# Kernel tuning notes

Hardware: AMD Instinct MI355X
Metric: run time of the kernel (lower is better)

## Reference

```python
import jax, jax.numpy as jnp
import numpy as np
import math
from jax import lax

B, D, L, K, CONV_NUM, NH, DK = 8, 128, 1024, 7, 4, 8, 16


def _pos_encoding():
    i = np.arange(D, dtype=np.float64)
    freqs = np.where(i % 2 == 0, 10000.0 ** (-i / D), -(10000.0 ** (-(i - 1) / D)))
    phases = np.where(i % 2 == 0, 0.0, math.pi / 2)
    pos = np.arange(L, dtype=np.float64)
    pe = np.sin(pos[None, :] * freqs[:, None] + phases[:, None])  # [D, L]
    return jnp.asarray(pe, dtype=jnp.float32)


def setup_inputs() -> dict:
    key = jax.random.key(0)
    ks = jax.random.split(key, 10)
    x = jax.random.normal(ks[0], (B, D, L), dtype=jnp.float32)
    pos_enc = _pos_encoding()
    ln_w = jnp.ones((D, L), dtype=jnp.float32)   # LayerNorm([D, L]) weight
    ln_b = jnp.zeros((D, L), dtype=jnp.float32)  # LayerNorm([D, L]) bias
    dw = jax.random.normal(ks[1], (CONV_NUM, D, K), dtype=jnp.float32) * 0.1   # depthwise kernels
    pw = jax.random.normal(ks[2], (CONV_NUM, D, D), dtype=jnp.float32) * 0.08  # pointwise (1x1) kernels
    Wq = jax.random.normal(ks[3], (NH, B, DK, D), dtype=jnp.float32) * 0.08
    Wk = jax.random.normal(ks[4], (NH, B, DK, D), dtype=jnp.float32) * 0.08
    Wv = jax.random.normal(ks[5], (NH, B, DK, D), dtype=jnp.float32) * 0.08
    Wo = jax.random.normal(ks[6], (B, D, D), dtype=jnp.float32) * 0.08
    W = jax.random.normal(ks[7], (B, D, D), dtype=jnp.float32) * 0.08
    return {"x": x, "pos_enc": pos_enc, "ln_w": ln_w, "ln_b": ln_b,
            "dw": dw, "pw": pw, "Wq": Wq, "Wk": Wk, "Wv": Wv, "Wo": Wo, "W": W}


def _layernorm(y, w, b):
    # normalized over the last two dims [D, L] (matches nn.LayerNorm([D, L]))
    m = jnp.mean(y, axis=(1, 2), keepdims=True)
    v = jnp.var(y, axis=(1, 2), keepdims=True)
    return (y - m) / jnp.sqrt(v + 1e-5) * w + b


def _dsconv(y, dwk, pwk):
    # depthwise conv1d (groups=D, padding=K//2, no bias), then pointwise 1x1
    y = lax.conv_general_dilated(
        y, dwk[:, None, :], window_strides=(1,), padding=[(K // 2, K // 2)],
        feature_group_count=D, dimension_numbers=("NCH", "OIH", "NCH"))
    return jnp.einsum("oc,bcl->bol", pwk, y)


def _self_attention(x, Wq, Wk, Wv, Wo):
    inv = 1.0 / math.sqrt(DK)
    Q = jnp.einsum("hbdc,bcl->hbdl", Wq, x)  # [NH,B,DK,L]
    Kt = jnp.einsum("hbdc,bcl->hbdl", Wk, x)
    V = jnp.einsum("hbdc,bcl->hbdl", Wv, x)
    scores = jnp.einsum("hbdl,hbdm->hblm", Q, Kt) * inv  # [NH,B,L,L]
    # torch does F.softmax(out, dim=1) on [B,L,L] -> softmax over the first L axis
    A = jax.nn.softmax(scores, axis=2)
    heads = jnp.einsum("hbvl,hblm->hbvm", V, A)  # [NH,B,DV,L]
    head = jnp.transpose(heads, (1, 0, 2, 3)).reshape(B, NH * DK, L)  # concat along channel dim
    return jnp.einsum("bdc,bcl->bdl", Wo, head)


def reference(x, pos_enc, ln_w, ln_b, dw, pw, Wq, Wk, Wv, Wo, W):
    # dropout layers are identity (eval mode)
    out = x + pos_enc[None, :, :]
    res = out
    for i in range(CONV_NUM):
        out = _layernorm(out, ln_w, ln_b)
        out = _dsconv(out, dw[i], pw[i])
        out = jax.nn.relu(out)
        out = out + res
        res = out
        out = _layernorm(out, ln_w, ln_b)
    out = _self_attention(out, Wq, Wk, Wv, Wo)
    out = out + res
    res = out
    out = _layernorm(out, ln_w, ln_b)
    out = jnp.einsum("bdc,bcl->bdl", W, out)
    out = jax.nn.relu(out)
    out = out + res
    return out
```

## Files before the change

kernel.cpp:

```cpp
#include <hip/hip_runtime.h>
#include <hip/hip_bf16.h>

#define B_ 8
#define D_ 128
#define L_ 1024
#define KSZ 7
#define NH_ 8
#define DK_ 16

constexpr int BD = D_ * L_;
constexpr float LN_EPS = 1e-5f;
constexpr float INV_N = 1.0f / (float)BD;

typedef _Float16 half4 __attribute__((ext_vector_type(4)));
typedef float f32x4 __attribute__((ext_vector_type(4)));

template<int NS>
__device__ __forceinline__ void block_reduce_wave(float* s, float* redbuf, float* slot, int tid) {
    #pragma unroll
    for (int k = 0; k < NS; ++k) {
        float v = s[k];
        #pragma unroll
        for (int mk = 32; mk >= 1; mk >>= 1) v += __shfl_xor(v, mk, 64);
        s[k] = v;
    }
    int w = tid >> 6, lane = tid & 63;
    __syncthreads();
    if (lane == 0) {
        #pragma unroll
        for (int k = 0; k < NS; ++k) redbuf[w * NS + k] = s[k];
    }
    __syncthreads();
    if (tid == 0) {
        #pragma unroll
        for (int k = 0; k < NS; ++k)
            slot[k] = redbuf[k] + redbuf[NS + k] + redbuf[2 * NS + k] + redbuf[3 * NS + k];
    }
}

template<int LNMODE>
__device__ __forceinline__ void ln_stats_wave0(
    const float* __restrict__ pin, const float* __restrict__ wmom,
    int b, float* stat4, int tid)
{
    if (tid < 64) {
        float s0=0,s1=0,s2=0,s3=0,s4=0,s5=0,w0=0,w1=0,w2=0,w3=0,w4=0;
        const float* p = pin + (b * 64 + tid) * 8;
        s0 = p[0]; s1 = p[1];
        if constexpr (LNMODE == 2) {
            s2 = p[2]; s3 = p[3]; s4 = p[4]; s5 = p[5];
            const float* q = wmom + tid * 8;
            w0 = q[0]; w1 = q[1]; w2 = q[2]; w3 = q[3]; w4 = q[4];
        }
        #pragma unroll
        for (int mk = 32; mk >= 1; mk >>= 1) {
            s0 += __shfl_xor(s0, mk, 64); s1 += __shfl_xor(s1, mk, 64);
            if constexpr (LNMODE == 2) {
                s2 += __shfl_xor(s2, mk, 64); s3 += __shfl_xor(s3, mk, 64);
                s4 += __shfl_xor(s4, mk, 64); s5 += __shfl_xor(s5, mk, 64);
                w0 += __shfl_xor(w0, mk, 64); w1 += __shfl_xor(w1, mk, 64);
                w2 += __shfl_xor(w2, mk, 64); w3 += __shfl_xor(w3, mk, 64);
                w4 += __shfl_xor(w4, mk, 64);
            }
        }
        if (tid == 0) {
            float m1 = s0 * INV_N;
            float r1 = rsqrtf(s1 * INV_N - m1 * m1 + LN_EPS);
            stat4[0] = m1; stat4[1] = r1;
            if constexpr (LNMODE == 2) {
                float Sy  = r1 * (s2 - m1 * w0) + w2;
                float Sy2 = r1 * r1 * (s4 - 2.f * m1 * s3 + m1 * m1 * w1)
                          + 2.f * r1 * (s5 - m1 * w4) + w3;
                float m2 = Sy * INV_N;
                float r2 = rsqrtf(Sy2 * INV_N - m2 * m2 + LN_EPS);
                stat4[2] = m2; stat4[3] = r2;
            }
        }
    }
    __syncthreads();
}

__global__ __launch_bounds__(256) void k_addpos_wm(
    const float* __restrict__ x, const float* __restrict__ pos,
    const float* __restrict__ lnw, const float* __restrict__ lnb,
    float* __restrict__ out, float* __restrict__ part, float* __restrict__ wp)
{
    __shared__ float red[32];
    int b = blockIdx.y, blk = blockIdx.x, tid = threadIdx.x;
    if (b == 8) {
        int base = blk * 2048 + tid * 8;
        float s[5] = {0.f, 0.f, 0.f, 0.f, 0.f};
        #pragma unroll
        for (int q = 0; q < 2; ++q) {
            float4 wv = *(const float4*)(lnw + base + q * 4);
            float4 bv = *(const float4*)(lnb + base + q * 4);
            float wa[4] = {wv.x, wv.y, wv.z, wv.w};
            float ba[4] = {bv.x, bv.y, bv.z, bv.w};
            #pragma unroll
            for (int e = 0; e < 4; ++e) {
                float w = wa[e], bb = ba[e];
                s[0] += w; s[1] += w * w; s[2] += bb; s[3] += bb * bb; s[4] += w * bb;
            }
        }
        block_reduce_wave<5>(s, red, wp + blk * 8, tid);
        return;
    }
    int base = b * BD + blk * 2048;
    const float4* x4 = (const float4*)(x + base);
    const float4* p4 = (const float4*)(pos + blk * 2048);
    float4* o4 = (float4*)(out + base);
    float s[2] = {0.f, 0.f};
    #pragma unroll
    for (int j = 0; j < 2; ++j) {
        int idx = j * 256 + tid;
        float4 xv = x4[idx], pv = p4[idx];
        float4 r = {xv.x + pv.x, xv.y + pv.y, xv.z + pv.z, xv.w + pv.w};
        o4[idx] = r;
        s[0] += r.x + r.y + r.z + r.w;
        s[1] += r.x * r.x + r.y * r.y + r.z * r.z + r.w * r.w;
    }
    block_reduce_wave<2>(s, red, part + (b * 64 + blk) * 8, tid);
}

template<int LNMODE>
__global__ __launch_bounds__(256) void k_convblock(
    const float* __restrict__ src, const float* __restrict__ lnw, const float* __restrict__ lnb,
    const float* __restrict__ dwk, const float* __restrict__ pwk,
    const float* __restrict__ wmom, const float* __restrict__ pin,
    float* __restrict__ outbuf, float* __restrict__ pout)
{
    constexpr int XSTR = 136;
    constexpr int CSTR = 20;
    __shared__ _Float16 Xt[16 * XSTR];
    __shared__ float Ct[128 * CSTR];
    __shared__ float stat4[4];
    __shared__ float red[32];
    int lt = blockIdx.x, b = blockIdx.y;
    int tid = threadIdx.x;
    int l0 = lt * 16;

    ln_stats_wave0<LNMODE>(pin, wmom, b, stat4, tid);
    float m1 = stat4[0], r1 = stat4[1];
    float m2 = 0.f, r2 = 1.f;
    if constexpr (LNMODE == 2) { m2 = stat4[2]; r2 = stat4[3]; }

    {
        int c = tid >> 1, lh = tid & 1;
        int base = l0 + lh * 8;
        const float* srow = src + b * BD + c * L_;
        const float* wrow = lnw + c * L_;
        const float* brow = lnb + c * L_;
        float z[16];
        #pragma unroll
        for (int q = 0; q < 4; ++q) {
            int le = base - 4 + q * 4;
            if (le >= 0 && le <= L_ - 4) {
                float4 sv = *(const float4*)(srow + le);
                float4 wv = *(const float4*)(wrow + le);
                float4 bv = *(const float4*)(brow + le);
                float sa[4] = {sv.x, sv.y, sv.z, sv.w};
                float wa[4] = {wv.x, wv.y, wv.z, wv.w};
                float ba[4] = {bv.x, bv.y, bv.z, bv.w};
                #pragma unroll
                for (int e = 0; e < 4; ++e) {
                    float y = (sa[e] - m1) * r1 * wa[e] + ba[e];
                    if constexpr (LNMODE == 2) y = (y - m2) * r2 * wa[e] + ba[e];
                    z[q * 4 + e] = y;
                }
            } else {
                #pragma unroll
                for (int e = 0; e < 4; ++e) {
                    int l = le + e;
                    float zz = 0.f;
                    if (l >= 0 && l < L_) {
                        float y = (srow[l] - m1) * r1 * wrow[l] + brow[l];
                        if constexpr (LNMODE == 2) y = (y - m2) * r2 * wrow[l] + brow[l];
                        zz = y;
                    }
                    z[q * 4 + e] = zz;
                }
            }
        }
        float t0 = dwk[c*KSZ+0], t1 = dwk[c*KSZ+1], t2 = dwk[c*KSZ+2], t3 = dwk[c*KSZ+3],
              t4 = dwk[c*KSZ+4], t5 = dwk[c*KSZ+5], t6 = dwk[c*KSZ+6];
        #pragma unroll
        for (int j = 0; j < 8; ++j) {
            float o = t0*z[j+1] + t1*z[j+2] + t2*z[j+3] + t3*z[j+4]
                    + t4*z[j+5] + t5*z[j+6] + t6*z[j+7];
            Xt[(lh * 8 + j) * XSTR + c] = (_Float16)o;
        }
    }
    __syncthreads();

    int w = tid >> 6, lane = tid & 63, lg = lane >> 4, ln = lane & 15;
    int o0 = w * 32;
    const float* wrow0 = pwk + (o0 + ln) * D_;
    const float* wrow1 = pwk + (o0 + 16 + ln) * D_;
    f32x4 acc0 = {0.f, 0.f, 0.f, 0.f};
    f32x4 acc1 = {0.f, 0.f, 0.f, 0.f};
    #pragma unroll
    for (int kk = 0; kk < 8; ++kk) {
        float4 wv0 = *(const float4*)(wrow0 + kk * 16 + lg * 4);
        float4 wv1 = *(const float4*)(wrow1 + kk * 16 + lg * 4);
        half4 af0 = {(_Float16)wv0.x, (_Float16)wv0.y, (_Float16)wv0.z, (_Float16)wv0.w};
        half4 af1 = {(_Float16)wv1.x, (_Float16)wv1.y, (_Float16)wv1.z, (_Float16)wv1.w};
        half4 bf = *(const half4*)(&Xt[ln * XSTR + kk * 16 + lg * 4]);
        acc0 = __builtin_amdgcn_mfma_f32_16x16x16f16(af0, bf, acc0, 0, 0, 0);
        acc1 = __builtin_amdgcn_mfma_f32_16x16x16f16(af1, bf, acc1, 0, 0, 0);
    }

    #pragma unroll
    for (int om = 0; om < 2; ++om) {
        const f32x4& a = om ? acc1 : acc0;
        #pragma unroll
        for (int r = 0; r < 4; ++r)
            Ct[(o0 + om * 16 + lg * 4 + r) * CSTR + ln] = a[r];
    }
    __syncthreads();

    float s[6] = {0.f, 0.f, 0.f, 0.f, 0.f, 0.f};
    {
        int og = tid >> 1, hh = tid & 1;
        int lcol = l0 + hh * 8;
        int idx = b * BD + og * L_ + lcol;
        int widx = og * L_ + lcol;
        float4 c0 = *(const float4*)(&Ct[og * CSTR + hh * 8]);
        float4 c1 = *(const float4*)(&Ct[og * CSTR + hh * 8 + 4]);
        float4 rs0 = *(const float4*)(src + idx);
        float4 rs1 = *(const float4*)(src + idx + 4);
        float4 w0 = *(const float4*)(lnw + widx);
        float4 w1 = *(const float4*)(lnw + widx + 4);
        float4 b0 = *(const float4*)(lnb + widx);
        float4 b1 = *(const float4*)(lnb + widx + 4);
        float cv[8] = {c0.x, c0.y, c0.z, c0.w, c1.x, c1.y, c1.z, c1.w};
        float rv[8] = {rs0.x, rs0.y, rs0.z, rs0.w, rs1.x, rs1.y, rs1.z, rs1.w};
        float wv[8] = {w0.x, w0.y, w0.z, w0.w, w1.x, w1.y, w1.z, w1.w};
        float bv[8] = {b0.x, b0.y, b0.z, b0.w, b1.x, b1.y, b1.z, b1.w};
        float ov[8];
        #pragma unroll
        for (int e = 0; e < 8; ++e) {
            float v = fmaxf(cv[e], 0.f) + rv[e];
            ov[e] = v;
            float wvv = wv[e] * v;
            s[0] += v; s[1] += v * v; s[2] += wvv;
            s[3] += wv[e] * wvv; s[4] += wvv * wvv; s[5] += bv[e] * wvv;
        }
        *(float4*)(outbuf + idx)     = (float4){ov[0], ov[1], ov[2], ov[3]};
        *(float4*)(outbuf + idx + 4) = (float4){ov[4], ov[5], ov[6], ov[7]};
    }
    block_reduce_wave<6>(s, red, pout + (b * 64 + lt) * 8, tid);
}

template<bool LNSTAGE, int XSTR>
__device__ __forceinline__ void stage_tile(
    const float* __restrict__ X, const float* __restrict__ lnw, const float* __restrict__ lnb,
    _Float16* Xt, int b, int l0, float m1, float r1, int tid)
{
    int c = tid >> 1, lh = tid & 1;
    int off = c * L_ + l0 + lh * 16;
    const float* xp = X + b * BD + off;
    const float* wp = lnw + off;
    const float* bp = lnb + off;
    #pragma unroll
    for (int q = 0; q < 4; ++q) {
        float4 v = *(const float4*)(xp + q * 4);
        if constexpr (LNSTAGE) {
            float4 wv = *(const float4*)(wp + q * 4);
            float4 bv = *(const float4*)(bp + q * 4);
            v.x = (v.x - m1) * r1 * wv.x + bv.x;
            v.y = (v.y - m1) * r1 * wv.y + bv.y;
            v.z = (v.z - m1) * r1 * wv.z + bv.z;
            v.w = (v.w - m1) * r1 * wv.w + bv.w;
        }
        int lb_ = lh * 16 + q * 4;
        Xt[(lb_ + 0) * XSTR + c] = (_Float16)v.x;
        Xt[(lb_ + 1) * XSTR + c] = (_Float16)v.y;
        Xt[(lb_ + 2) * XSTR + c] = (_Float16)v.z;
        Xt[(lb_ + 3) * XSTR + c] = (_Float16)v.w;
    }
}

__global__ __launch_bounds__(256) void k_qkv(
    const float* __restrict__ Wq, const float* __restrict__ Wk, const float* __restrict__ Wv,
    const float* __restrict__ X, const float* __restrict__ lnw, const float* __restrict__ lnb,
    const float* __restrict__ pin,
    float* __restrict__ oq, float* __restrict__ ok, float* __restrict__ ov)
{
    constexpr int XSTR = 136;
    constexpr int CSTR = 36;
    __shared__ _Float16 Xt[32 * XSTR];
    __shared__ float Ct[64 * CSTR];
    __shared__ float stat4[4];
    int lt = blockIdx.x, rb = blockIdx.y, b = blockIdx.z;
    int tid = threadIdx.x;
    int l0 = lt * 32, r0 = rb * 64;

    ln_stats_wave0<1>(pin, nullptr, b, stat4, tid);
    stage_tile<true, XSTR>(X, lnw, lnb, Xt, b, l0, stat4[0], stat4[1], tid);
    __syncthreads();

    int w = tid >> 6, lane = tid & 63, lg = lane >> 4, ln = lane & 15;
    int o = r0 + w * 16 + ln;
    int woff = (o >> 4) * (B_ * DK_ * D_) + b * (DK_ * D_) + (o & 15) * D_;

    half4 bf[2][8];
    #pragma unroll
    for (int n = 0; n < 2; ++n)
        #pragma unroll
        for (int kk = 0; kk < 8; ++kk)
            bf[n][kk] = *(const half4*)(&Xt[(n * 16 + ln) * XSTR + kk * 16 + lg * 4]);

    const float* Wms[3] = {Wq, Wk, Wv};
    float* outs[3] = {oq, ok, ov};
    #pragma unroll
    for (int g = 0; g < 3; ++g) {
        const float* wrow = Wms[g] + woff;
        f32x4 acc0 = {0.f, 0.f, 0.f, 0.f};
        f32x4 acc1 = {0.f, 0.f, 0.f, 0.f};
        #pragma unroll
        for (int kk = 0; kk < 8; ++kk) {
            float4 wv = *(const float4*)(wrow + kk * 16 + lg * 4);
            half4 af = {(_Float16)wv.x, (_Float16)wv.y, (_Float16)wv.z, (_Float16)wv.w};
            acc0 = __builtin_amdgcn_mfma_f32_16x16x16f16(af, bf[0][kk], acc0, 0, 0, 0);
            acc1 = __builtin_amdgcn_mfma_f32_16x16x16f16(af, bf[1][kk], acc1, 0, 0, 0);
        }
        if (g) __syncthreads();
        #pragma unroll
        for (int n = 0; n < 2; ++n) {
            const f32x4& a = n ? acc1 : acc0;
            #pragma unroll
            for (int r = 0; r < 4; ++r)
                Ct[(w * 16 + lg * 4 + r) * CSTR + n * 16 + ln] = a[r];
        }
        __syncthreads();
        int row = tid >> 2, q4 = tid & 3;
        int og = r0 + row, lcol = l0 + q4 * 8;
        float4 c0 = *(const float4*)(&Ct[row * CSTR + q4 * 8]);
        float4 c1 = *(const float4*)(&Ct[row * CSTR + q4 * 8 + 4]);
        int idx = b * BD + og * L_ + lcol;
        *(float4*)(outs[g] + idx)     = c0;
        *(float4*)(outs[g] + idx + 4) = c1;
    }
}

template<bool RELU, bool ADDRES, bool STATS, bool LNSTAGE>
__global__ __launch_bounds__(256) void k_matmul_mfma(
    const float* __restrict__ Wm, const float* __restrict__ X,
    const float* __restrict__ lnw, const float* __restrict__ lnb,
    const float* __restrict__ pin,
    const float* __restrict__ res, float* __restrict__ out, float* __restrict__ part)
{
    constexpr int XSTR = 136;
    constexpr int CSTR = 36;
    __shared__ _Float16 Xt[32 * XSTR];
    __shared__ float Ct[64 * CSTR];
    __shared__ float stat4[4];
    __shared__ float red[32];
    int lt = blockIdx.x, rb = blockIdx.y, b = blockIdx.z;
    int tid = threadIdx.x;
    int l0 = lt * 32, r0 = rb * 64;

    if constexpr (LNSTAGE) ln_stats_wave0<1>(pin, nullptr, b, stat4, tid);
    float m1 = LNSTAGE ? stat4[0] : 0.f, r1 = LNSTAGE ? stat4[1] : 1.f;
    stage_tile<LNSTAGE, XSTR>(X, lnw, lnb, Xt, b, l0, m1, r1, tid);
    __syncthreads();

    int w = tid >> 6, lane = tid & 63, lg = lane >> 4, ln = lane & 15;
    int o = r0 + w * 16 + ln;
    const float* wrow = Wm + b * D_ * D_ + o * D_;

    f32x4 acc0 = {0.f, 0.f, 0.f, 0.f};
    f32x4 acc1 = {0.f, 0.f, 0.f, 0.f};
    #pragma unroll
    for (int kk = 0; kk < 8; ++kk) {
        float4 wv = *(const float4*)(wrow + kk * 16 + lg * 4);
        half4 af = {(_Float16)wv.x, (_Float16)wv.y, (_Float16)wv.z, (_Float16)wv.w};
        half4 b0 = *(const half4*)(&Xt[ln * XSTR + kk * 16 + lg * 4]);
        half4 b1 = *(const half4*)(&Xt[(16 + ln) * XSTR + kk * 16 + lg * 4]);
        acc0 = __builtin_amdgcn_mfma_f32_16x16x16f16(af, b0, acc0, 0, 0, 0);
        acc1 = __builtin_amdgcn_mfma_f32_16x16x16f16(af, b1, acc1, 0, 0, 0);
    }

    #pragma unroll
    for (int n = 0; n < 2; ++n) {
        const f32x4& a = n ? acc1 : acc0;
        #pragma unroll
        for (int r = 0; r < 4; ++r)
            Ct[(w * 16 + lg * 4 + r) * CSTR + n * 16 + ln] = a[r];
    }
    __syncthreads();

    float s[2] = {0.f, 0.f};
    {
        int row = tid >> 2, q4 = tid & 3;
        int og = r0 + row, lcol = l0 + q4 * 8;
        int idx = b * BD + og * L_ + lcol;
        float4 c0 = *(const float4*)(&Ct[row * CSTR + q4 * 8]);
        float4 c1 = *(const float4*)(&Ct[row * CSTR + q4 * 8 + 4]);
        float cv[8] = {c0.x, c0.y, c0.z, c0.w, c1.x, c1.y, c1.z, c1.w};
        float rv[8] = {0.f, 0.f, 0.f, 0.f, 0.f, 0.f, 0.f, 0.f};
        if constexpr (ADDRES) {
            float4 r0v = *(const float4*)(res + idx);
            float4 r1v = *(const float4*)(res + idx + 4);
            rv[0]=r0v.x; rv[1]=r0v.y; rv[2]=r0v.z; rv[3]=r0v.w;
            rv[4]=r1v.x; rv[5]=r1v.y; rv[6]=r1v.z; rv[7]=r1v.w;
        }
        float ov[8];
        #pragma unroll
        for (int e = 0; e < 8; ++e) {
            float v = cv[e];
            if constexpr (RELU) v = fmaxf(v, 0.f);
            v += rv[e];
            ov[e] = v;
            if constexpr (STATS) { s[0] += v; s[1] += v * v; }
        }
        *(float4*)(out + idx)     = (float4){ov[0], ov[1], ov[2], ov[3]};
        *(float4*)(out + idx + 4) = (float4){ov[4], ov[5], ov[6], ov[7]};
    }
    if constexpr (STATS) block_reduce_wave<2>(s, red, part + (b * 64 + rb * 32 + lt) * 8, tid);
}

__global__ __launch_bounds__(256) void k_attn_mfma(
    const float* __restrict__ Qb, const float* __restrict__ Kb,
    const float* __restrict__ Vb, float* __restrict__ outb)
{
    constexpr int QSTR = 20;
    constexpr int VSTR = 72;
    constexpr int OSTR = 68;
    __shared__ _Float16 Qs[2][64 * QSTR];
    __shared__ _Float16 Vs[2][16 * VSTR];
    __shared__ float Ot[16 * OSTR];
    int mt = blockIdx.x, h = blockIdx.y, b = blockIdx.z;
    int tid = threadIdx.x;
    int w = tid >> 6, lane = tid & 63, lg = lane >> 4, ln = lane & 15;
    int m = mt * 64 + w * 16 + ln;
    const float* Qp = Qb + b * BD + (h * DK_) * L_;
    const float* Kp = Kb + b * BD + (h * DK_) * L_;
    const float* Vp = Vb + b * BD + (h * DK_) * L_;

    half4 kfrag;
    #pragma unroll
    for (int j = 0; j < 4; ++j)
        kfrag[j] = (_Float16)(Kp[(lg * 4 + j) * L_ + m] * 0.25f);

    f32x4 accf[4];
    #pragma unroll
    for (int f = 0; f < 4; ++f) accf[f] = (f32x4){0.f, 0.f, 0.f, 0.f};
    float run_sm = 0.f;

    int sd = tid >> 4, slq = tid & 15;
    const float* qsrc = Qp + sd * L_ + slq * 4;
    const float* vsrc = Vp + sd * L_ + slq * 4;
    float4 qv = *(const float4*)(qsrc);
    float4 vv = *(const float4*)(vsrc);

    for (int lt = 0; lt < 16; ++lt) {
        int cb = lt & 1;
        Qs[cb][(slq*4+0)*QSTR + sd] = (_Float16)qv.x;
        Qs[cb][(slq*4+1)*QSTR + sd] = (_Float16)qv.y;
        Qs[cb][(slq*4+2)*QSTR + sd] = (_Float16)qv.z;
        Qs[cb][(slq*4+3)*QSTR + sd] = (_Float16)qv.w;
        half4 vh = {(_Float16)vv.x, (_Float16)vv.y, (_Float16)vv.z, (_Float16)vv.w};
        *(half4*)(&Vs[cb][sd * VSTR + slq * 4]) = vh;
        __syncthreads();
        if (lt < 15) {
            qv = *(const float4*)(qsrc + (lt + 1) * 64);
            vv = *(const float4*)(vsrc + (lt + 1) * 64);
        }

        f32x4 s[4];
        #pragma unroll
        for (int f = 0; f < 4; ++f) {
            half4 qfrag = *(const half4*)(&Qs[cb][(f * 16 + ln) * QSTR + lg * 4]);
            f32x4 z = {0.f, 0.f, 0.f, 0.f};
            s[f] = __builtin_amdgcn_mfma_f32_16x16x16f16(qfrag, kfrag, z, 0, 0, 0);
        }

        float ts = 0.f;
        half4 pf[4];
        #pragma unroll
        for (int f = 0; f < 4; ++f) {
            float p0 = __expf(s[f][0]);
            float p1 = __expf(s[f][1]);
            float p2 = __expf(s[f][2]);
            float p3 = __expf(s[f][3]);
            ts += (p0 + p1) + (p2 + p3);
            pf[f][0] = (_Float16)p0; pf[f][1] = (_Float16)p1;
            pf[f][2] = (_Float16)p2; pf[f][3] = (_Float16)p3;
        }
        ts += __shfl_xor(ts, 16, 64);
        ts += __shfl_xor(ts, 32, 64);
        run_sm += ts;

        #pragma unroll
        for (int f = 0; f < 4; ++f) {
            half4 vfrag = *(const half4*)(&Vs[cb][ln * VSTR + f * 16 + lg * 4]);
            accf[f] = __builtin_amdgcn_mfma_f32_16x16x16f16(vfrag, pf[f], accf[f], 0, 0, 0);
        }
    }

    float inv = 1.f / run_sm;
    #pragma unroll
    for (int r = 0; r < 4; ++r) {
        float a = (accf[0][r] + accf[1][r]) + (accf[2][r] + accf[3][r]);
        Ot[(lg * 4 + r) * OSTR + w * 16 + ln] = a * inv;
    }
    __syncthreads();
    {
        int row = tid >> 4, col = (tid & 15) * 4;
        float4 o4 = *(const float4*)(&Ot[row * OSTR + col]);
        *(float4*)(outb + b * BD + (h * DK_ + row) * L_ + mt * 64 + col) = o4;
    }
}


extern "C" void kernel_launch(void* const* d_in, const int* in_sizes, int n_in,
                              void* d_out, int out_size, void* d_ws, size_t ws_size,
                              hipStream_t stream)
{
    const float* x   = (const float*)d_in[0];
    const float* pos = (const float*)d_in[1];
    const float* lnw = (const float*)d_in[2];
    const float* lnb = (const float*)d_in[3];
    const float* dw  = (const float*)d_in[4];
    const float* pw  = (const float*)d_in[5];
    const float* Wq  = (const float*)d_in[6];
    const float* Wk  = (const float*)d_in[7];
    const float* Wv  = (const float*)d_in[8];
    const float* Wo  = (const float*)d_in[9];
    const float* Wf  = (const float*)d_in[10];
    float* out = (float*)d_out;

    float* ws = (float*)d_ws;
    float* WP = ws;
    float* P0 = ws + 512;
    float* P1 = P0 + 4096;
    float* P2 = P1 + 4096;
    float* P3 = P2 + 4096;
    float* P4 = P3 + 4096;
    float* P5 = P4 + 4096;
    float* bufA  = ws + 32768;
    float* bufB  = bufA + (size_t)B_ * BD;
    float* buf_q = bufB + (size_t)B_ * BD;
    float* buf_k = buf_q + (size_t)B_ * BD;
    float* buf_v = buf_k + (size_t)B_ * BD;

    dim3 cb(64, 8);
    dim3 mb(32, 2, 8);

    k_addpos_wm<<<dim3(64, 9), 256, 0, stream>>>(x, pos, lnw, lnb, bufA, P0, WP);

    k_convblock<1><<<cb, 256, 0, stream>>>(bufA, lnw, lnb, dw + 0*D_*KSZ, pw + 0*D_*D_, WP, P0, bufB, P1);
    k_convblock<2><<<cb, 256, 0, stream>>>(bufB, lnw, lnb, dw + 1*D_*KSZ, pw + 1*D_*D_, WP, P1, bufA, P2);
    k_convblock<2><<<cb, 256, 0, stream>>>(bufA, lnw, lnb, dw + 2*D_*KSZ, pw + 2*D_*D_, WP, P2, bufB, P3);
    k_convblock<2><<<cb, 256, 0, stream>>>(bufB, lnw, lnb, dw + 3*D_*KSZ, pw + 3*D_*D_, WP, P3, bufA, P4);

    k_qkv<<<mb, 256, 0, stream>>>(Wq, Wk, Wv, bufA, lnw, lnb, P4, buf_q, buf_k, buf_v);

    k_attn_mfma<<<dim3(16, NH_, B_), 256, 0, stream>>>(buf_q, buf_k, buf_v, bufB);

    k_matmul_mfma<false, true, true, false><<<mb, 256, 0, stream>>>(Wo, bufB, lnw, lnb, nullptr, bufA, buf_q, P5);
    k_matmul_mfma<true, true, false, true><<<mb, 256, 0, stream>>>(Wf, buf_q, lnw, lnb, P5, buf_q, out, nullptr);
}
```

Before: 113.2 us.

## Store Q/K/V and attention output as fp16 in MFMA-friendly layouts

```diff
diff --git a/kernel.cpp b/kernel.cpp
--- a/kernel.cpp
+++ b/kernel.cpp
@@ -13,6 +13,7 @@
 constexpr float INV_N = 1.0f / (float)BD;
 
 typedef _Float16 half4 __attribute__((ext_vector_type(4)));
+typedef _Float16 half8 __attribute__((ext_vector_type(8)));
 typedef float f32x4 __attribute__((ext_vector_type(4)));
 
 template<int NS>
@@ -284,7 +285,7 @@
     const float* __restrict__ Wq, const float* __restrict__ Wk, const float* __restrict__ Wv,
     const float* __restrict__ X, const float* __restrict__ lnw, const float* __restrict__ lnb,
     const float* __restrict__ pin,
-    float* __restrict__ oq, float* __restrict__ ok, float* __restrict__ ov)
+    _Float16* __restrict__ Qt, _Float16* __restrict__ Kt, _Float16* __restrict__ Vh)
 {
     constexpr int XSTR = 136;
     constexpr int CSTR = 36;
@@ -311,7 +312,6 @@
             bf[n][kk] = *(const half4*)(&Xt[(n * 16 + ln) * XSTR + kk * 16 + lg * 4]);
 
     const float* Wms[3] = {Wq, Wk, Wv};
-    float* outs[3] = {oq, ok, ov};
     #pragma unroll
     for (int g = 0; g < 3; ++g) {
         const float* wrow = Wms[g] + woff;
@@ -333,14 +333,154 @@
                 Ct[(w * 16 + lg * 4 + r) * CSTR + n * 16 + ln] = a[r];
         }
         __syncthreads();
+        if (g < 2) {
+            int hd = tid >> 6, lrel = (tid >> 1) & 31, hf = tid & 1;
+            int h = rb * 4 + hd, l = l0 + lrel;
+            half8 hv;
+            #pragma unroll
+            for (int k = 0; k < 8; ++k)
+                hv[k] = (_Float16)Ct[(hd * 16 + hf * 8 + k) * CSTR + lrel];
+            _Float16* dst = (g == 0 ? Qt : Kt);
+            *(half8*)(dst + ((b * NH_ + h) * L_ + l) * 16 + hf * 8) = hv;
+        } else {
+            int row = tid >> 2, q4 = tid & 3;
+            int h = rb * 4 + (row >> 4), v = row & 15;
+            float4 c0 = *(const float4*)(&Ct[row * CSTR + q4 * 8]);
+            float4 c1 = *(const float4*)(&Ct[row * CSTR + q4 * 8 + 4]);
+            half8 hv = {(_Float16)c0.x, (_Float16)c0.y, (_Float16)c0.z, (_Float16)c0.w,
+                        (_Float16)c1.x, (_Float16)c1.y, (_Float16)c1.z, (_Float16)c1.w};
+            *(half8*)(Vh + ((b * NH_ + h) * DK_ + v) * L_ + l0 + q4 * 8) = hv;
+        }
+    }
+}
+
+__global__ __launch_bounds__(256) void k_attn_mfma(
+    const _Float16* __restrict__ Qt, const _Float16* __restrict__ Kt,
+    const _Float16* __restrict__ Vh, _Float16* __restrict__ H16)
+{
+    __shared__ _Float16 Om[64 * 16];
+    int mt = blockIdx.x, h = blockIdx.y, b = blockIdx.z;
+    int tid = threadIdx.x;
+    int w = tid >> 6, lane = tid & 63, lg = lane >> 4, ln = lane & 15;
+    int m = mt * 64 + w * 16 + ln;
+    const _Float16* Qh = Qt + (b * NH_ + h) * L_ * 16;
+    const _Float16* Kh = Kt + (b * NH_ + h) * L_ * 16;
+    const _Float16* Vp = Vh + (b * NH_ + h) * DK_ * L_;
+
+    half4 kraw = *(const half4*)(Kh + m * 16 + lg * 4);
+    half4 kfrag;
+    #pragma unroll
+    for (int j = 0; j < 4; ++j) kfrag[j] = kraw[j] * (_Float16)0.25f;
+
+    f32x4 accf[4];
+    #pragma unroll
+    for (int f = 0; f < 4; ++f) accf[f] = (f32x4){0.f, 0.f, 0.f, 0.f};
+    float run_sm = 0.f;
+
+    for (int lt = 0; lt < 16; ++lt) {
+        int l0 = lt * 64;
+        f32x4 s[4];
+        #pragma unroll
+        for (int f = 0; f < 4; ++f) {
+            half4 qf = *(const half4*)(Qh + (l0 + f * 16 + ln) * 16 + lg * 4);
+            f32x4 z = {0.f, 0.f, 0.f, 0.f};
+            s[f] = __builtin_amdgcn_mfma_f32_16x16x16f16(qf, kfrag, z, 0, 0, 0);
+        }
+        float ts = 0.f;
+        half4 pf[4];
+        #pragma unroll
+        for (int f = 0; f < 4; ++f) {
+            float p0 = __expf(s[f][0]);
+            float p1 = __expf(s[f][1]);
+            float p2 = __expf(s[f][2]);
+            float p3 = __expf(s[f][3]);
+            ts += (p0 + p1) + (p2 + p3);
+            pf[f][0] = (_Float16)p0; pf[f][1] = (_Float16)p1;
+            pf[f][2] = (_Float16)p2; pf[f][3] = (_Float16)p3;
+        }
+        ts += __shfl_xor(ts, 16, 64);
+        ts += __shfl_xor(ts, 32, 64);
+        run_sm += ts;
+        #pragma unroll
+        for (int f = 0; f < 4; ++f) {
+            half4 vf = *(const half4*)(Vp + ln * L_ + l0 + f * 16 + lg * 4);
+            accf[f] = __builtin_amdgcn_mfma_f32_16x16x16f16(vf, pf[f], accf[f], 0, 0, 0);
+        }
+    }
+
+    float inv = 1.f / run_sm;
+    #pragma unroll
+    for (int r = 0; r < 4; ++r) {
+        float a = (accf[0][r] + accf[1][r]) + (accf[2][r] + accf[3][r]);
+        Om[(w * 16 + ln) * 16 + lg * 4 + r] = (_Float16)(a * inv);
+    }
+    __syncthreads();
+    if (tid < 128) {
+        int ml = tid >> 1, hf = tid & 1;
+        half8 hv = *(const half8*)(&Om[ml * 16 + hf * 8]);
+        *(half8*)(H16 + (b * L_ + mt * 64 + ml) * 128 + h * 16 + hf * 8) = hv;
+    }
+}
+
+__global__ __launch_bounds__(256) void k_matmul_h16(
+    const float* __restrict__ Wm, const _Float16* __restrict__ H16,
+    const float* __restrict__ res, float* __restrict__ out, float* __restrict__ part)
+{
+    constexpr int CSTR = 36;
+    __shared__ float Ct[64 * CSTR];
+    __shared__ float red[32];
+    int lt = blockIdx.x, rb = blockIdx.y, b = blockIdx.z;
+    int tid = threadIdx.x;
+    int l0 = lt * 32, r0 = rb * 64;
+
+    int w = tid >> 6, lane = tid & 63, lg = lane >> 4, ln = lane & 15;
+    int o = r0 + w * 16 + ln;
+    const float* wrow = Wm + b * D_ * D_ + o * D_;
+    const _Float16* Hb = H16 + (size_t)b * L_ * 128;
+
+    f32x4 acc0 = {0.f, 0.f, 0.f, 0.f};
+    f32x4 acc1 = {0.f, 0.f, 0.f, 0.f};
+    #pragma unroll
+    for (int kk = 0; kk < 8; ++kk) {
+        float4 wv = *(const float4*)(wrow + kk * 16 + lg * 4);
+        half4 af = {(_Float16)wv.x, (_Float16)wv.y, (_Float16)wv.z, (_Float16)wv.w};
+        half4 b0 = *(const half4*)(Hb + (l0 + ln) * 128 + kk * 16 + lg * 4);
+        half4 b1 = *(const half4*)(Hb + (l0 + 16 + ln) * 128 + kk * 16 + lg * 4);
+        acc0 = __builtin_amdgcn_mfma_f32_16x16x16f16(af, b0, acc0, 0, 0, 0);
+        acc1 = __builtin_amdgcn_mfma_f32_16x16x16f16(af, b1, acc1, 0, 0, 0);
+    }
+
+    #pragma unroll
+    for (int n = 0; n < 2; ++n) {
+        const f32x4& a = n ? acc1 : acc0;
+        #pragma unroll
+        for (int r = 0; r < 4; ++r)
+            Ct[(w * 16 + lg * 4 + r) * CSTR + n * 16 + ln] = a[r];
+    }
+    __syncthreads();
+
+    float s[2] = {0.f, 0.f};
+    {
         int row = tid >> 2, q4 = tid & 3;
         int og = r0 + row, lcol = l0 + q4 * 8;
+        int idx = b * BD + og * L_ + lcol;
         float4 c0 = *(const float4*)(&Ct[row * CSTR + q4 * 8]);
         float4 c1 = *(const float4*)(&Ct[row * CSTR + q4 * 8 + 4]);
-        int idx = b * BD + og * L_ + lcol;
-        *(float4*)(outs[g] + idx)     = c0;
-        *(float4*)(outs[g] + idx + 4) = c1;
-    }
+        float4 r0v = *(const float4*)(res + idx);
+        float4 r1v = *(const float4*)(res + idx + 4);
+        float cv[8] = {c0.x, c0.y, c0.z, c0.w, c1.x, c1.y, c1.z, c1.w};
+        float rv[8] = {r0v.x, r0v.y, r0v.z, r0v.w, r1v.x, r1v.y, r1v.z, r1v.w};
+        float ov[8];
+        #pragma unroll
+        for (int e = 0; e < 8; ++e) {
+            float v = cv[e] + rv[e];
+            ov[e] = v;
+            s[0] += v; s[1] += v * v;
+        }
+        *(float4*)(out + idx)     = (float4){ov[0], ov[1], ov[2], ov[3]};
+        *(float4*)(out + idx + 4) = (float4){ov[4], ov[5], ov[6], ov[7]};
+    }
+    block_reduce_wave<2>(s, red, part + (b * 64 + rb * 32 + lt) * 8, tid);
 }
 
 template<bool RELU, bool ADDRES, bool STATS, bool LNSTAGE>
@@ -420,99 +560,6 @@
     if constexpr (STATS) block_reduce_wave<2>(s, red, part + (b * 64 + rb * 32 + lt) * 8, tid);
 }
 
-__global__ __launch_bounds__(256) void k_attn_mfma(
-    const float* __restrict__ Qb, const float* __restrict__ Kb,
-    const float* __restrict__ Vb, float* __restrict__ outb)
-{
-    constexpr int QSTR = 20;
-    constexpr int VSTR = 72;
-    constexpr int OSTR = 68;
-    __shared__ _Float16 Qs[2][64 * QSTR];
-    __shared__ _Float16 Vs[2][16 * VSTR];
-    __shared__ float Ot[16 * OSTR];
-    int mt = blockIdx.x, h = blockIdx.y, b = blockIdx.z;
-    int tid = threadIdx.x;
-    int w = tid >> 6, lane = tid & 63, lg = lane >> 4, ln = lane & 15;
-    int m = mt * 64 + w * 16 + ln;
-    const float* Qp = Qb + b * BD + (h * DK_) * L_;
-    const float* Kp = Kb + b * BD + (h * DK_) * L_;
-    const float* Vp = Vb + b * BD + (h * DK_) * L_;
-
-    half4 kfrag;
-    #pragma unroll
-    for (int j = 0; j < 4; ++j)
-        kfrag[j] = (_Float16)(Kp[(lg * 4 + j) * L_ + m] * 0.25f);
-
-    f32x4 accf[4];
-    #pragma unroll
-    for (int f = 0; f < 4; ++f) accf[f] = (f32x4){0.f, 0.f, 0.f, 0.f};
-    float run_sm = 0.f;
-
-    int sd = tid >> 4, slq = tid & 15;
-    const float* qsrc = Qp + sd * L_ + slq * 4;
-    const float* vsrc = Vp + sd * L_ + slq * 4;
-    float4 qv = *(const float4*)(qsrc);
-    float4 vv = *(const float4*)(vsrc);
-
-    for (int lt = 0; lt < 16; ++lt) {
-        int cb = lt & 1;
-        Qs[cb][(slq*4+0)*QSTR + sd] = (_Float16)qv.x;
-        Qs[cb][(slq*4+1)*QSTR + sd] = (_Float16)qv.y;
-        Qs[cb][(slq*4+2)*QSTR + sd] = (_Float16)qv.z;
-        Qs[cb][(slq*4+3)*QSTR + sd] = (_Float16)qv.w;
-        half4 vh = {(_Float16)vv.x, (_Float16)vv.y, (_Float16)vv.z, (_Float16)vv.w};
-        *(half4*)(&Vs[cb][sd * VSTR + slq * 4]) = vh;
-        __syncthreads();
-        if (lt < 15) {
-            qv = *(const float4*)(qsrc + (lt + 1) * 64);
-            vv = *(const float4*)(vsrc + (lt + 1) * 64);
-        }
-
-        f32x4 s[4];
-        #pragma unroll
-        for (int f = 0; f < 4; ++f) {
-            half4 qfrag = *(const half4*)(&Qs[cb][(f * 16 + ln) * QSTR + lg * 4]);
-            f32x4 z = {0.f, 0.f, 0.f, 0.f};
-            s[f] = __builtin_amdgcn_mfma_f32_16x16x16f16(qfrag, kfrag, z, 0, 0, 0);
-        }
-
-        float ts = 0.f;
-        half4 pf[4];
-        #pragma unroll
-        for (int f = 0; f < 4; ++f) {
-            float p0 = __expf(s[f][0]);
-            float p1 = __expf(s[f][1]);
-            float p2 = __expf(s[f][2]);
-            float p3 = __expf(s[f][3]);
-            ts += (p0 + p1) + (p2 + p3);
-            pf[f][0] = (_Float16)p0; pf[f][1] = (_Float16)p1;
-            pf[f][2] = (_Float16)p2; pf[f][3] = (_Float16)p3;
-        }
-        ts += __shfl_xor(ts, 16, 64);
-        ts += __shfl_xor(ts, 32, 64);
-        run_sm += ts;
-
-        #pragma unroll
-        for (int f = 0; f < 4; ++f) {
-            half4 vfrag = *(const half4*)(&Vs[cb][ln * VSTR + f * 16 + lg * 4]);
-            accf[f] = __builtin_amdgcn_mfma_f32_16x16x16f16(vfrag, pf[f], accf[f], 0, 0, 0);
-        }
-    }
-
-    float inv = 1.f / run_sm;
-    #pragma unroll
-    for (int r = 0; r < 4; ++r) {
-        float a = (accf[0][r] + accf[1][r]) + (accf[2][r] + accf[3][r]);
-        Ot[(lg * 4 + r) * OSTR + w * 16 + ln] = a * inv;
-    }
-    __syncthreads();
-    {
-        int row = tid >> 4, col = (tid & 15) * 4;
-        float4 o4 = *(const float4*)(&Ot[row * OSTR + col]);
-        *(float4*)(outb + b * BD + (h * DK_ + row) * L_ + mt * 64 + col) = o4;
-    }
-}
-
 
 extern "C" void kernel_launch(void* const* d_in, const int* in_sizes, int n_in,
                               void* d_out, int out_size, void* d_ws, size_t ws_size,
@@ -539,11 +586,13 @@
     float* P3 = P2 + 4096;
     float* P4 = P3 + 4096;
     float* P5 = P4 + 4096;
-    float* bufA  = ws + 32768;
-    float* bufB  = bufA + (size_t)B_ * BD;
-    float* buf_q = bufB + (size_t)B_ * BD;
-    float* buf_k = buf_q + (size_t)B_ * BD;
-    float* buf_v = buf_k + (size_t)B_ * BD;
+    float* bufA = ws + 32768;
+    float* bufB = bufA + (size_t)B_ * BD;
+    float* bufC = bufB + (size_t)B_ * BD;
+    _Float16* Qt  = (_Float16*)(bufC + (size_t)B_ * BD);
+    _Float16* Kt  = Qt + (size_t)B_ * NH_ * L_ * 16;
+    _Float16* Vh  = Kt + (size_t)B_ * NH_ * L_ * 16;
+    _Float16* H16 = Vh + (size_t)B_ * NH_ * DK_ * L_;
 
     dim3 cb(64, 8);
     dim3 mb(32, 2, 8);
@@ -555,10 +604,10 @@
     k_convblock<2><<<cb, 256, 0, stream>>>(bufA, lnw, lnb, dw + 2*D_*KSZ, pw + 2*D_*D_, WP, P2, bufB, P3);
     k_convblock<2><<<cb, 256, 0, stream>>>(bufB, lnw, lnb, dw + 3*D_*KSZ, pw + 3*D_*D_, WP, P3, bufA, P4);
 
-    k_qkv<<<mb, 256, 0, stream>>>(Wq, Wk, Wv, bufA, lnw, lnb, P4, buf_q, buf_k, buf_v);
-
-    k_attn_mfma<<<dim3(16, NH_, B_), 256, 0, stream>>>(buf_q, buf_k, buf_v, bufB);
-
-    k_matmul_mfma<false, true, true, false><<<mb, 256, 0, stream>>>(Wo, bufB, lnw, lnb, nullptr, bufA, buf_q, P5);
-    k_matmul_mfma<true, true, false, true><<<mb, 256, 0, stream>>>(Wf, buf_q, lnw, lnb, P5, buf_q, out, nullptr);
-}
+    k_qkv<<<mb, 256, 0, stream>>>(Wq, Wk, Wv, bufA, lnw, lnb, P4, Qt, Kt, Vh);
+
+    k_attn_mfma<<<dim3(16, NH_, B_), 256, 0, stream>>>(Qt, Kt, Vh, H16);
+
+    k_matmul_h16<<<mb, 256, 0, stream>>>(Wo, H16, bufA, bufC, P5);
+    k_matmul_mfma<true, true, false, true><<<mb, 256, 0, stream>>>(Wf, bufC, lnw, lnb, P5, bufC, out, nullptr);
+}
```

After: 131.9 us. +16.5%, slower.
